# Optimization experiments

Measured on AMD Instinct MI355X. Metric: run time of the kernel, lower is better.

The kernel has to match this reference:

```python
import jax, jax.numpy as jnp
import numpy as np

D_MODEL = 2048
N_HEADS = 16
HEAD_DIM = 128
WINDOW = 512
ROPE_BASE = 10000.0
B, N = 2, 2048
INNER = N_HEADS * HEAD_DIM


def setup_inputs() -> dict:
    key = jax.random.key(0)
    k1, k2, k3 = jax.random.split(key, 3)
    x = jax.random.normal(k1, (B, N, D_MODEL), dtype=jnp.float32)
    # torch nn.Linear stores weight as [out_features, in_features]
    w_qkv = jax.random.normal(k2, (3 * INNER, D_MODEL), dtype=jnp.float32) / np.sqrt(D_MODEL)
    w_o = jax.random.normal(k3, (D_MODEL, INNER), dtype=jnp.float32) / np.sqrt(INNER)
    return {"x": x, "w_qkv": w_qkv, "w_o": w_o}


def _rotate_half(t):
    t1, t2 = jnp.split(t, 2, axis=-1)
    return jnp.concatenate([-t2, t1], axis=-1)


def _rope(q, k, offset=0):
    # q, k: [B, H, N, D]; GPT-NeoX half-split rotary embedding
    D = q.shape[-1]
    inv_freq = 1.0 / (ROPE_BASE ** (jnp.arange(0, D, 2, dtype=jnp.float32) / D))
    pos = jnp.arange(q.shape[2], dtype=jnp.float32) + offset
    ang = pos[:, None] * inv_freq[None, :]                 # [N, D/2]
    cos = jnp.concatenate([jnp.cos(ang), jnp.cos(ang)], axis=-1)  # [N, D]
    sin = jnp.concatenate([jnp.sin(ang), jnp.sin(ang)], axis=-1)
    q_r = q * cos + _rotate_half(q) * sin
    k_r = k * cos + _rotate_half(k) * sin
    return q_r, k_r


def reference(x, w_qkv, w_o):
    Bq, Nq, _ = x.shape
    # QKV projection (no bias)
    qkv = jnp.einsum('bnd,ed->bne', x, w_qkv)              # [B, N, 3*INNER]
    q, k, v = jnp.split(qkv, 3, axis=-1)
    def to_heads(t):
        return t.reshape(Bq, Nq, N_HEADS, HEAD_DIM).transpose(0, 2, 1, 3)  # [B,H,N,D]
    q, k, v = to_heads(q), to_heads(k), to_heads(v)
    q, k = _rope(q, k, offset=0)
    # sliding-window causal mask: valid key j for query i iff (i - WINDOW) < j <= i
    i = jnp.arange(Nq)[:, None]
    j = jnp.arange(Nq)[None, :]
    valid = (j > i - WINDOW) & (j <= i)                    # [N, N]
    scale = 1.0 / np.sqrt(HEAD_DIM)
    scores = jnp.einsum('bhnd,bhkd->bhnk', q, k) * scale   # [B,H,N,N]
    scores = jnp.where(valid[None, None], scores, -jnp.inf)
    att = jax.nn.softmax(scores, axis=-1)
    out = jnp.einsum('bhnk,bhkd->bhnd', att, v)
    out = out.transpose(0, 2, 1, 3).reshape(Bq, Nq, INNER)
    y = jnp.einsum('bni,di->bnd', out, w_o)
    return y
```

## Files before the change

### kernel.cpp

```cpp
#include <hip/hip_runtime.h>
#include <hip/hip_bf16.h>
#include <cstdint>

typedef __bf16 bf16x8 __attribute__((ext_vector_type(8)));
typedef float floatx4 __attribute__((ext_vector_type(4)));

__device__ __forceinline__ void gl2lds16(const void* g, void* l) {
  __builtin_amdgcn_global_load_lds(
      (const __attribute__((address_space(1))) unsigned int*)g,
      (__attribute__((address_space(3))) unsigned int*)(uintptr_t)l,
      16, 0, 0);
}

__global__ __launch_bounds__(256)
void cvt_kernel(const float* __restrict__ in, __hip_bfloat16* __restrict__ out, int n) {
  int i = (blockIdx.x * 256 + threadIdx.x) * 4;
  if (i >= n) return;
  const float4 v = *(const float4*)(in + i);
  out[i + 0] = __float2bfloat16(v.x);
  out[i + 1] = __float2bfloat16(v.y);
  out[i + 2] = __float2bfloat16(v.z);
  out[i + 3] = __float2bfloat16(v.w);
}

__global__ __launch_bounds__(256)
void cvt2_kernel(const float* __restrict__ in0, const float* __restrict__ in1,
                 __hip_bfloat16* __restrict__ out, int n0, int ntot) {
  int i = (blockIdx.x * 256 + threadIdx.x) * 4;
  if (i >= ntot) return;
  const float4 v = (i < n0) ? *(const float4*)(in0 + i)
                            : *(const float4*)(in1 + (i - n0));
  out[i + 0] = __float2bfloat16(v.x);
  out[i + 1] = __float2bfloat16(v.y);
  out[i + 2] = __float2bfloat16(v.z);
  out[i + 3] = __float2bfloat16(v.w);
}

#define MEMFENCE asm volatile("" ::: "memory")

__global__ __launch_bounds__(512, 2)
void gemm_qkv256(const __hip_bfloat16* __restrict__ A,
                 const __hip_bfloat16* __restrict__ W,
                 __hip_bfloat16* __restrict__ Qr,
                 __hip_bfloat16* __restrict__ Kr,
                 __hip_bfloat16* __restrict__ Vt)
{
  extern __shared__ __hip_bfloat16 sm[];
  const int tid = threadIdx.x, lane = tid & 63, wave = tid >> 6;
  const int wr = wave >> 2, wc = wave & 3;
  const int m0 = blockIdx.x << 8, n0 = blockIdx.y << 8;
  const int lrow = lane & 15, dg = lane >> 4, lq4 = dg * 4;
  const int rslot = (dg ^ ((lrow >> 1) & 3)) * 8;
  const int arow = tid >> 2;
  const int ascol = ((tid & 3) ^ ((tid >> 3) & 3)) * 8;
  const __hip_bfloat16* aS0 = A + (size_t)(m0 + arow) * 2048 + ascol;
  const __hip_bfloat16* aS1 = A + (size_t)(m0 + 128 + arow) * 2048 + ascol;
  const __hip_bfloat16* bS0 = W + (size_t)(n0 + arow) * 2048 + ascol;
  const __hip_bfloat16* bS1 = W + (size_t)(n0 + 128 + arow) * 2048 + ascol;
  floatx4 acc[8][4] = {};

#define QSTAGE(TT) do { const int bb_ = (TT) & 3; const int kk_ = (TT) * 32;   \
    gl2lds16(aS0 + kk_, &sm[bb_ * 16384 + tid * 8]);                           \
    gl2lds16(aS1 + kk_, &sm[bb_ * 16384 + 4096 + tid * 8]);                    \
    gl2lds16(bS0 + kk_, &sm[bb_ * 16384 + 8192 + tid * 8]);                    \
    gl2lds16(bS1 + kk_, &sm[bb_ * 16384 + 12288 + tid * 8]); } while (0)

#define QKSTEP(TT, WIMM, DOSTAGE) do {                                         \
    MEMFENCE; __builtin_amdgcn_s_waitcnt(WIMM); MEMFENCE;                      \
    __builtin_amdgcn_s_barrier(); MEMFENCE;                                    \
    const int bb = (TT) & 3;                                                   \
    if (DOSTAGE) QSTAGE((TT) + 3);                                             \
    bf16x8 af[8], bfr[4];                                                      \
    _Pragma("unroll")                                                          \
    for (int mt = 0; mt < 8; mt++)                                             \
      af[mt] = *(const bf16x8*)&sm[bb * 16384 + (wr * 128 + mt * 16 + lrow) * 32 + rslot]; \
    _Pragma("unroll")                                                          \
    for (int nt = 0; nt < 4; nt++)                                             \
      bfr[nt] = *(const bf16x8*)&sm[bb * 16384 + 8192 + (wc * 64 + nt * 16 + lrow) * 32 + rslot]; \
    __builtin_amdgcn_s_setprio(1);                                             \
    _Pragma("unroll")                                                          \
    for (int mt = 0; mt < 8; mt++)                                             \
      _Pragma("unroll")                                                        \
      for (int nt = 0; nt < 4; nt++)                                           \
        acc[mt][nt] = __builtin_amdgcn_mfma_f32_16x16x32_bf16(af[mt], bfr[nt], acc[mt][nt], 0, 0, 0); \
    __builtin_amdgcn_s_setprio(0);                                             \
  } while (0)

  QSTAGE(0); QSTAGE(1); QSTAGE(2);
  for (int t = 0; t < 61; ++t) QKSTEP(t, 0x0078, true);
  QKSTEP(61, 0x0078, false);
  QKSTEP(62, 0x0074, false);
  QKSTEP(63, 0x0070, false);
#undef QKSTEP
#undef QSTAGE

  const int seg = n0 >> 11;
  const int h0 = (n0 & 2047) >> 7;
  const int b = m0 >> 11;
  const int seq0 = m0 & 2047;
  float* invfp = (float*)((char*)sm + 122880);

  __syncthreads();
  if (seg < 2 && tid < 64) invfp[tid] = __expf(-(float)tid * 0.14391156831212787f);

  const float qs = (seg == 0) ? 0.08838834764831845f : 1.0f;
  for (int p = 0; p < 2; ++p) {
    if (p) __syncthreads();
    if (wr == p) {
      if (seg < 2) {
#pragma unroll
        for (int mt = 0; mt < 8; mt++)
#pragma unroll
          for (int nt = 0; nt < 4; nt++)
#pragma unroll
            for (int r = 0; r < 4; r++)
              sm[(mt * 16 + lq4 + r) * 264 + wc * 64 + nt * 16 + lrow] =
                  __float2bfloat16(acc[mt][nt][r]);
      } else {
#pragma unroll
        for (int mt = 0; mt < 8; mt++)
#pragma unroll
          for (int nt = 0; nt < 4; nt++)
#pragma unroll
            for (int r = 0; r < 4; r++)
              sm[(wc * 64 + nt * 16 + lrow) * 136 + mt * 16 + lq4 + r] =
                  __float2bfloat16(acc[mt][nt][r]);
      }
    }
    __syncthreads();
    if (seg < 2) {
      __hip_bfloat16* Out = seg ? Kr : Qr;
#pragma unroll
      for (int it = 0; it < 4; ++it) {
        const int task = tid + it * 512;
        const int row = task >> 4;
        const int hh = (task >> 3) & 1;
        const int g8 = (task & 7) * 8;
        const int seq = seq0 + p * 128 + row;
        const float pos = (float)seq;
        const bf16x8 lo8 = *(const bf16x8*)&sm[row * 264 + hh * 128 + g8];
        const bf16x8 hi8 = *(const bf16x8*)&sm[row * 264 + hh * 128 + g8 + 64];
        alignas(16) __hip_bfloat16 lo[8], hi[8];
#pragma unroll
        for (int k = 0; k < 8; k++) {
          float sn, cs;
          __sincosf(pos * invfp[g8 + k], &sn, &cs);
          const float a = (float)lo8[k];
          const float bb2 = (float)hi8[k];
          lo[k] = __float2bfloat16((a * cs - bb2 * sn) * qs);
          hi[k] = __float2bfloat16((bb2 * cs + a * sn) * qs);
        }
        const size_t ob = ((size_t)((b * 16 + h0 + hh) * 2048 + seq)) * 128;
        *(bf16x8*)&Out[ob + g8] = *(const bf16x8*)lo;
        *(bf16x8*)&Out[ob + g8 + 64] = *(const bf16x8*)hi;
      }
    } else {
#pragma unroll
      for (int it = 0; it < 8; ++it) {
        const int task = tid + it * 512;
        const int col = task >> 4;
        const int sg = (task & 15) * 8;
        const bf16x8 v8 = *(const bf16x8*)&sm[col * 136 + sg];
        const int hh = col >> 7, d = col & 127;
        *(bf16x8*)&Vt[((size_t)((b * 16 + h0 + hh) * 128 + d)) * 2048 + seq0 + p * 128 + sg] = v8;
      }
    }
  }
}

__global__ __launch_bounds__(512, 2)
void gemm_o256(const __hip_bfloat16* __restrict__ A,
               const __hip_bfloat16* __restrict__ Wo,
               float* __restrict__ C)
{
  extern __shared__ __hip_bfloat16 sm[];
  const int tid = threadIdx.x, lane = tid & 63, wave = tid >> 6;
  const int wr = wave >> 2, wc = wave & 3;
  const int m0 = blockIdx.x << 8, n0 = blockIdx.y << 7;
  const int lrow = lane & 15, dg = lane >> 4, lq4 = dg * 4;
  const int rslot = (dg ^ ((lrow >> 1) & 3)) * 8;
  const int arow = tid >> 2;
  const int ascol = ((tid & 3) ^ ((tid >> 3) & 3)) * 8;
  const __hip_bfloat16* aS0 = A + (size_t)(m0 + arow) * 2048 + ascol;
  const __hip_bfloat16* aS1 = A + (size_t)(m0 + 128 + arow) * 2048 + ascol;
  const __hip_bfloat16* bS0 = Wo + (size_t)(n0 + arow) * 2048 + ascol;
  floatx4 acc[8][2] = {};

#define OSTAGE(TT) do { const int bb_ = (TT) & 3; const int kk_ = (TT) * 32;   \
    gl2lds16(aS0 + kk_, &sm[bb_ * 12288 + tid * 8]);                           \
    gl2lds16(aS1 + kk_, &sm[bb_ * 12288 + 4096 + tid * 8]);                    \
    gl2lds16(bS0 + kk_, &sm[bb_ * 12288 + 8192 + tid * 8]); } while (0)

#define OKSTEP(TT, WIMM, DOSTAGE) do {                                         \
    MEMFENCE; __builtin_amdgcn_s_waitcnt(WIMM); MEMFENCE;                      \
    __builtin_amdgcn_s_barrier(); MEMFENCE;                                    \
    const int bb = (TT) & 3;                                                   \
    if (DOSTAGE) OSTAGE((TT) + 3);                                             \
    bf16x8 af[8], bfr[2];                                                      \
    _Pragma("unroll")                                                          \
    for (int mt = 0; mt < 8; mt++)                                             \
      af[mt] = *(const bf16x8*)&sm[bb * 12288 + (wr * 128 + mt * 16 + lrow) * 32 + rslot]; \
    _Pragma("unroll")                                                          \
    for (int nt = 0; nt < 2; nt++)                                             \
      bfr[nt] = *(const bf16x8*)&sm[bb * 12288 + 8192 + (wc * 32 + nt * 16 + lrow) * 32 + rslot]; \
    __builtin_amdgcn_s_setprio(1);                                             \
    _Pragma("unroll")                                                          \
    for (int mt = 0; mt < 8; mt++)                                             \
      _Pragma("unroll")                                                        \
      for (int nt = 0; nt < 2; nt++)                                           \
        acc[mt][nt] = __builtin_amdgcn_mfma_f32_16x16x32_bf16(af[mt], bfr[nt], acc[mt][nt], 0, 0, 0); \
    __builtin_amdgcn_s_setprio(0);                                             \
  } while (0)

  OSTAGE(0); OSTAGE(1); OSTAGE(2);
  for (int t = 0; t < 61; ++t) OKSTEP(t, 0x0076, true);
  OKSTEP(61, 0x0076, false);
  OKSTEP(62, 0x0073, false);
  OKSTEP(63, 0x0070, false);
#undef OKSTEP
#undef OSTAGE

#pragma unroll
  for (int mt = 0; mt < 8; mt++)
#pragma unroll
    for (int nt = 0; nt < 2; nt++)
#pragma unroll
      for (int r = 0; r < 4; r++)
        C[(size_t)(m0 + wr * 128 + mt * 16 + lq4 + r) * 2048 +
          (n0 + wc * 32 + nt * 16 + lrow)] = acc[mt][nt][r];
}

#define KSTR 136
#define VSTR 72
__global__ __launch_bounds__(512, 4)
void attn_swa(const __hip_bfloat16* __restrict__ Qr, const __hip_bfloat16* __restrict__ Kr,
              const __hip_bfloat16* __restrict__ Vt, __hip_bfloat16* __restrict__ Out)
{
  __shared__ __hip_bfloat16 Ks[64 * KSTR];
  __shared__ __hip_bfloat16 Vs[128 * VSTR];
  __shared__ __hip_bfloat16 Pb[8][16 * VSTR];
  const int qt = blockIdx.x, bh = blockIdx.y;
  const int tid = threadIdx.x, lane = tid & 63, wave = tid >> 6;
  const int lrow = lane & 15, lk = (lane >> 4) * 8, lq4 = (lane >> 4) * 4;
  const int i0 = qt * 128;
  const float NEG_INF = -__builtin_inff();
  const __hip_bfloat16* Qh = Qr + (size_t)bh * 2048 * 128;
  const __hip_bfloat16* Kh = Kr + (size_t)bh * 2048 * 128;
  const __hip_bfloat16* Vh = Vt + (size_t)bh * 128 * 2048;

  const int ck0 = tid, ck1 = tid + 512;
  const int kr0 = ck0 >> 4, kg0 = (ck0 & 15) * 8;
  const int kr1 = ck1 >> 4, kg1 = (ck1 & 15) * 8;
  const int cv0 = tid, cv1 = tid + 512;
  const int vd0 = cv0 >> 3, vc0 = (cv0 & 7) * 8;
  const int vd1 = cv1 >> 3, vc1 = (cv1 & 7) * 8;

  const int iw = i0 + wave * 16 + lrow;
  bf16x8 qf[4];
#pragma unroll
  for (int ks = 0; ks < 4; ks++)
    qf[ks] = *(const bf16x8*)&Qh[(size_t)iw * 128 + ks * 32 + lk];

  floatx4 accO[8] = {};
  float m_i = NEG_INF, l_i = 0.f;
  const int imin = i0 + wave * 16;
  const int lo = i0 - 511;
  const int jt_lo = (lo > 0 ? lo : 0) >> 6;
  const int jt_hi = (i0 + 127) >> 6;

  int j0n = jt_lo * 64;
  int4 rk0 = *(const int4*)&Kh[(size_t)(j0n + kr0) * 128 + kg0];
  int4 rk1 = *(const int4*)&Kh[(size_t)(j0n + kr1) * 128 + kg1];
  int4 rv0 = *(const int4*)&Vh[(size_t)vd0 * 2048 + j0n + vc0];
  int4 rv1 = *(const int4*)&Vh[(size_t)vd1 * 2048 + j0n + vc1];

  for (int jt = jt_lo; jt <= jt_hi; jt++) {
    const int j0 = jt * 64;
    __syncthreads();
    *(int4*)&Ks[kr0 * KSTR + kg0] = rk0;
    *(int4*)&Ks[kr1 * KSTR + kg1] = rk1;
    *(int4*)&Vs[vd0 * VSTR + vc0] = rv0;
    *(int4*)&Vs[vd1 * VSTR + vc1] = rv1;
    if (jt < jt_hi) {
      const int jn = j0 + 64;
      rk0 = *(const int4*)&Kh[(size_t)(jn + kr0) * 128 + kg0];
      rk1 = *(const int4*)&Kh[(size_t)(jn + kr1) * 128 + kg1];
      rv0 = *(const int4*)&Vh[(size_t)vd0 * 2048 + jn + vc0];
      rv1 = *(const int4*)&Vh[(size_t)vd1 * 2048 + jn + vc1];
    }
    asm volatile("" ::: "memory");
    __builtin_amdgcn_s_waitcnt(0xC07F);
    __builtin_amdgcn_s_barrier();
    asm volatile("" ::: "memory");

    floatx4 s[4] = {};
#pragma unroll
    for (int nt = 0; nt < 4; nt++) {
      const int krow = (nt * 16 + lrow) * KSTR;
#pragma unroll
      for (int ks = 0; ks < 4; ks++) {
        const bf16x8 kf = *(const bf16x8*)&Ks[krow + ks * 32 + lk];
        s[nt] = __builtin_amdgcn_mfma_f32_16x16x32_bf16(kf, qf[ks], s[nt], 0, 0, 0);
      }
    }
    const bool full = (j0 + 63 <= imin) && (j0 >= imin + 15 - 511);
    float rmax = NEG_INF;
    if (full) {
#pragma unroll
      for (int nt = 0; nt < 4; nt++)
#pragma unroll
        for (int r = 0; r < 4; r++) rmax = fmaxf(rmax, s[nt][r]);
    } else {
#pragma unroll
      for (int nt = 0; nt < 4; nt++) {
#pragma unroll
        for (int r = 0; r < 4; r++) {
          const int j = j0 + nt * 16 + lq4 + r;
          const float sv = ((j <= iw) && (j > iw - 512)) ? s[nt][r] : NEG_INF;
          s[nt][r] = sv;
          rmax = fmaxf(rmax, sv);
        }
      }
    }
    rmax = fmaxf(rmax, __shfl_xor(rmax, 16));
    rmax = fmaxf(rmax, __shfl_xor(rmax, 32));
    const float mnew = fmaxf(m_i, rmax);
    const float alpha = __expf(fminf(m_i - mnew, 0.f));
    m_i = mnew;
    float rs = 0.f;
    if (full) {
#pragma unroll
      for (int nt = 0; nt < 4; nt++)
#pragma unroll
        for (int r = 0; r < 4; r++) {
          const float p = __expf(s[nt][r] - mnew);
          s[nt][r] = p;
          rs += p;
        }
    } else {
#pragma unroll
      for (int nt = 0; nt < 4; nt++)
#pragma unroll
        for (int r = 0; r < 4; r++) {
          const float sv = s[nt][r];
          const float p = (sv == NEG_INF) ? 0.f : __expf(sv - mnew);
          s[nt][r] = p;
          rs += p;
        }
    }
    rs += __shfl_xor(rs, 16);
    rs += __shfl_xor(rs, 32);
    l_i = l_i * alpha + rs;
#pragma unroll
    for (int dt = 0; dt < 8; dt++) accO[dt] *= alpha;
#pragma unroll
    for (int nt = 0; nt < 4; nt++) {
      alignas(8) __hip_bfloat16 p4[4];
#pragma unroll
      for (int r = 0; r < 4; r++) p4[r] = __float2bfloat16(s[nt][r]);
      *(uint64_t*)&Pb[wave][lrow * VSTR + nt * 16 + lq4] = *(const uint64_t*)p4;
    }
    bf16x8 pf[2];
#pragma unroll
    for (int jf = 0; jf < 2; jf++)
      pf[jf] = *(const bf16x8*)&Pb[wave][lrow * VSTR + jf * 32 + lk];
#pragma unroll
    for (int dt = 0; dt < 8; dt++) {
      const int vrow = (dt * 16 + lrow) * VSTR;
#pragma unroll
      for (int jf = 0; jf < 2; jf++) {
        const bf16x8 vf = *(const bf16x8*)&Vs[vrow + jf * 32 + lk];
        accO[dt] = __builtin_amdgcn_mfma_f32_16x16x32_bf16(vf, pf[jf], accO[dt], 0, 0, 0);
      }
    }
  }
  const int b = bh >> 4, h = bh & 15;
  const float inv_l = 1.0f / l_i;
  const size_t rowb = ((size_t)(b * 2048 + iw)) * 2048 + h * 128;
#pragma unroll
  for (int dt = 0; dt < 8; dt++) {
    alignas(8) __hip_bfloat16 o4[4];
#pragma unroll
    for (int r = 0; r < 4; r++) o4[r] = __float2bfloat16(accO[dt][r] * inv_l);
    *(uint64_t*)&Out[rowb + dt * 16 + lq4] = *(const uint64_t*)o4;
  }
}

extern "C" void kernel_launch(void* const* d_in, const int* in_sizes, int n_in,
                              void* d_out, int out_size, void* d_ws, size_t ws_size,
                              hipStream_t stream)
{
  const float* x = (const float*)d_in[0];
  const float* w_qkv = (const float*)d_in[1];
  const float* w_o = (const float*)d_in[2];
  float* y = (float*)d_out;
  char* ws = (char*)d_ws;

  const size_t SZ_X = 16777216;
  const size_t SZ_WQKV = 25165824;
  const size_t SZ_Q = 16777216;

  __hip_bfloat16* xb = (__hip_bfloat16*)(ws);
  __hip_bfloat16* wqkvb = (__hip_bfloat16*)(ws + SZ_X);
  __hip_bfloat16* Qr = (__hip_bfloat16*)(ws + SZ_X + SZ_WQKV);
  __hip_bfloat16* Kr = (__hip_bfloat16*)(ws + SZ_X + SZ_WQKV + SZ_Q);
  __hip_bfloat16* Vt = (__hip_bfloat16*)(ws + SZ_X + SZ_WQKV + 2 * SZ_Q);

  static bool s_attr_done = false;
  if (!s_attr_done) {
    hipFuncSetAttribute((const void*)gemm_qkv256,
                        hipFuncAttributeMaxDynamicSharedMemorySize, 131072);
    hipFuncSetAttribute((const void*)gemm_o256,
                        hipFuncAttributeMaxDynamicSharedMemorySize, 98304);
    s_attr_done = true;
  }

  cvt2_kernel<<<dim3(20480), dim3(256), 0, stream>>>(x, w_qkv, xb, 8388608, 20971520);
  gemm_qkv256<<<dim3(16, 24), dim3(512), 131072, stream>>>(xb, wqkvb, Qr, Kr, Vt);
  attn_swa<<<dim3(16, 32), dim3(512), 0, stream>>>(Qr, Kr, Vt, xb );
  cvt_kernel<<<dim3(4096), dim3(256), 0, stream>>>(w_o, wqkvb, 4194304);
  gemm_o256<<<dim3(16, 16), dim3(512), 98304, stream>>>(xb, wqkvb, y);
}
```

Baseline: 338.9 us.

## Shrink QKV GEMM tile to 128x128 with swizzled block order and 3-stage pipeline

Rewrites the QKV projection GEMM from 256x256 tiles with 512 threads and a 4-stage LDS ring to 128x128 tiles with 256 threads and a 3-stage ring. Block IDs are remapped with an XCD-style swizzle for L2 locality, and the epilogue now handles a single head per block. The aim is more blocks (1536 instead of 384) and more resident blocks per CU, to fill the GPU better and reduce tail effects. The cost is lower arithmetic intensity per tile, so more global/L2 traffic for A and W.

```diff
diff --git a/kernel.cpp b/kernel.cpp
--- a/kernel.cpp
+++ b/kernel.cpp
@@ -38,8 +38,8 @@
 
 #define MEMFENCE asm volatile("" ::: "memory")
 
-__global__ __launch_bounds__(512, 2)
-void gemm_qkv256(const __hip_bfloat16* __restrict__ A,
+__global__ __launch_bounds__(256, 3)
+void gemm_qkv128(const __hip_bfloat16* __restrict__ A,
                  const __hip_bfloat16* __restrict__ W,
                  __hip_bfloat16* __restrict__ Qr,
                  __hip_bfloat16* __restrict__ Kr,
@@ -47,123 +47,118 @@
 {
   extern __shared__ __hip_bfloat16 sm[];
   const int tid = threadIdx.x, lane = tid & 63, wave = tid >> 6;
-  const int wr = wave >> 2, wc = wave & 3;
-  const int m0 = blockIdx.x << 8, n0 = blockIdx.y << 8;
+  const int wr = wave >> 1, wc = wave & 1;
+  const int bid = blockIdx.y * 32 + blockIdx.x;
+  const int swz = (bid & 7) * 192 + (bid >> 3);
+  const int m0 = (swz & 31) << 7;
+  const int n0 = (swz >> 5) << 7;
   const int lrow = lane & 15, dg = lane >> 4, lq4 = dg * 4;
   const int rslot = (dg ^ ((lrow >> 1) & 3)) * 8;
   const int arow = tid >> 2;
   const int ascol = ((tid & 3) ^ ((tid >> 3) & 3)) * 8;
   const __hip_bfloat16* aS0 = A + (size_t)(m0 + arow) * 2048 + ascol;
-  const __hip_bfloat16* aS1 = A + (size_t)(m0 + 128 + arow) * 2048 + ascol;
+  const __hip_bfloat16* aS1 = A + (size_t)(m0 + 64 + arow) * 2048 + ascol;
   const __hip_bfloat16* bS0 = W + (size_t)(n0 + arow) * 2048 + ascol;
-  const __hip_bfloat16* bS1 = W + (size_t)(n0 + 128 + arow) * 2048 + ascol;
-  floatx4 acc[8][4] = {};
-
-#define QSTAGE(TT) do { const int bb_ = (TT) & 3; const int kk_ = (TT) * 32;   \
-    gl2lds16(aS0 + kk_, &sm[bb_ * 16384 + tid * 8]);                           \
-    gl2lds16(aS1 + kk_, &sm[bb_ * 16384 + 4096 + tid * 8]);                    \
-    gl2lds16(bS0 + kk_, &sm[bb_ * 16384 + 8192 + tid * 8]);                    \
-    gl2lds16(bS1 + kk_, &sm[bb_ * 16384 + 12288 + tid * 8]); } while (0)
-
-#define QKSTEP(TT, WIMM, DOSTAGE) do {                                         \
-    MEMFENCE; __builtin_amdgcn_s_waitcnt(WIMM); MEMFENCE;                      \
-    __builtin_amdgcn_s_barrier(); MEMFENCE;                                    \
-    const int bb = (TT) & 3;                                                   \
-    if (DOSTAGE) QSTAGE((TT) + 3);                                             \
-    bf16x8 af[8], bfr[4];                                                      \
-    _Pragma("unroll")                                                          \
-    for (int mt = 0; mt < 8; mt++)                                             \
-      af[mt] = *(const bf16x8*)&sm[bb * 16384 + (wr * 128 + mt * 16 + lrow) * 32 + rslot]; \
+  const __hip_bfloat16* bS1 = W + (size_t)(n0 + 64 + arow) * 2048 + ascol;
+  float* invfp = (float*)((char*)sm + 49152);
+  if (tid < 64) invfp[tid] = __expf(-(float)tid * 0.14391156831212787f);
+  floatx4 acc[4][4] = {};
+
+#define QS128(TT) do { const int bo_ = ((TT) % 3) * 8192; const int kk_ = (TT) * 32; \
+    gl2lds16(aS0 + kk_, &sm[bo_ + tid * 8]);                                   \
+    gl2lds16(aS1 + kk_, &sm[bo_ + 2048 + tid * 8]);                            \
+    gl2lds16(bS0 + kk_, &sm[bo_ + 4096 + tid * 8]);                            \
+    gl2lds16(bS1 + kk_, &sm[bo_ + 6144 + tid * 8]); } while (0)
+
+#define QC128(BO) do {                                                         \
+    bf16x8 af[4], bfr[4];                                                      \
+    _Pragma("unroll")                                                          \
+    for (int mt = 0; mt < 4; mt++)                                             \
+      af[mt] = *(const bf16x8*)&sm[(BO) + (wr * 64 + mt * 16 + lrow) * 32 + rslot]; \
     _Pragma("unroll")                                                          \
     for (int nt = 0; nt < 4; nt++)                                             \
-      bfr[nt] = *(const bf16x8*)&sm[bb * 16384 + 8192 + (wc * 64 + nt * 16 + lrow) * 32 + rslot]; \
+      bfr[nt] = *(const bf16x8*)&sm[(BO) + 4096 + (wc * 64 + nt * 16 + lrow) * 32 + rslot]; \
     __builtin_amdgcn_s_setprio(1);                                             \
     _Pragma("unroll")                                                          \
-    for (int mt = 0; mt < 8; mt++)                                             \
+    for (int mt = 0; mt < 4; mt++)                                             \
       _Pragma("unroll")                                                        \
       for (int nt = 0; nt < 4; nt++)                                           \
         acc[mt][nt] = __builtin_amdgcn_mfma_f32_16x16x32_bf16(af[mt], bfr[nt], acc[mt][nt], 0, 0, 0); \
     __builtin_amdgcn_s_setprio(0);                                             \
   } while (0)
 
-  QSTAGE(0); QSTAGE(1); QSTAGE(2);
-  for (int t = 0; t < 61; ++t) QKSTEP(t, 0x0078, true);
-  QKSTEP(61, 0x0078, false);
-  QKSTEP(62, 0x0074, false);
-  QKSTEP(63, 0x0070, false);
-#undef QKSTEP
-#undef QSTAGE
+  QS128(0); QS128(1);
+  for (int t = 0; t < 63; ++t) {
+    MEMFENCE; __builtin_amdgcn_s_waitcnt(0x0074); MEMFENCE;
+    __builtin_amdgcn_s_barrier(); MEMFENCE;
+    if (t < 62) QS128(t + 2);
+    QC128((t % 3) * 8192);
+  }
+  MEMFENCE; __builtin_amdgcn_s_waitcnt(0x0070); MEMFENCE;
+  __builtin_amdgcn_s_barrier(); MEMFENCE;
+  QC128((63 % 3) * 8192);
+#undef QC128
+#undef QS128
 
   const int seg = n0 >> 11;
-  const int h0 = (n0 & 2047) >> 7;
+  const int h = (n0 & 2047) >> 7;
   const int b = m0 >> 11;
   const int seq0 = m0 & 2047;
-  float* invfp = (float*)((char*)sm + 122880);
-
   __syncthreads();
-  if (seg < 2 && tid < 64) invfp[tid] = __expf(-(float)tid * 0.14391156831212787f);
-
+  if (seg < 2) {
+#pragma unroll
+    for (int mt = 0; mt < 4; mt++)
+#pragma unroll
+      for (int nt = 0; nt < 4; nt++)
+#pragma unroll
+        for (int r = 0; r < 4; r++)
+          sm[(wr * 64 + mt * 16 + lq4 + r) * 136 + wc * 64 + nt * 16 + lrow] =
+              __float2bfloat16(acc[mt][nt][r]);
+  } else {
+#pragma unroll
+    for (int mt = 0; mt < 4; mt++)
+#pragma unroll
+      for (int nt = 0; nt < 4; nt++)
+#pragma unroll
+        for (int r = 0; r < 4; r++)
+          sm[(wc * 64 + nt * 16 + lrow) * 136 + wr * 64 + mt * 16 + lq4 + r] =
+              __float2bfloat16(acc[mt][nt][r]);
+  }
+  __syncthreads();
   const float qs = (seg == 0) ? 0.08838834764831845f : 1.0f;
-  for (int p = 0; p < 2; ++p) {
-    if (p) __syncthreads();
-    if (wr == p) {
-      if (seg < 2) {
-#pragma unroll
-        for (int mt = 0; mt < 8; mt++)
-#pragma unroll
-          for (int nt = 0; nt < 4; nt++)
-#pragma unroll
-            for (int r = 0; r < 4; r++)
-              sm[(mt * 16 + lq4 + r) * 264 + wc * 64 + nt * 16 + lrow] =
-                  __float2bfloat16(acc[mt][nt][r]);
-      } else {
-#pragma unroll
-        for (int mt = 0; mt < 8; mt++)
-#pragma unroll
-          for (int nt = 0; nt < 4; nt++)
-#pragma unroll
-            for (int r = 0; r < 4; r++)
-              sm[(wc * 64 + nt * 16 + lrow) * 136 + mt * 16 + lq4 + r] =
-                  __float2bfloat16(acc[mt][nt][r]);
+  if (seg < 2) {
+    __hip_bfloat16* Out = seg ? Kr : Qr;
+#pragma unroll
+    for (int it = 0; it < 4; ++it) {
+      const int task = tid + it * 256;
+      const int row = task >> 3;
+      const int g8 = (task & 7) * 8;
+      const int seq = seq0 + row;
+      const float pos = (float)seq;
+      const bf16x8 lo8 = *(const bf16x8*)&sm[row * 136 + g8];
+      const bf16x8 hi8 = *(const bf16x8*)&sm[row * 136 + g8 + 64];
+      alignas(16) __hip_bfloat16 lo[8], hi[8];
+#pragma unroll
+      for (int k = 0; k < 8; k++) {
+        float sn, cs;
+        __sincosf(pos * invfp[g8 + k], &sn, &cs);
+        const float a = (float)lo8[k];
+        const float bb2 = (float)hi8[k];
+        lo[k] = __float2bfloat16((a * cs - bb2 * sn) * qs);
+        hi[k] = __float2bfloat16((bb2 * cs + a * sn) * qs);
       }
-    }
-    __syncthreads();
-    if (seg < 2) {
-      __hip_bfloat16* Out = seg ? Kr : Qr;
-#pragma unroll
-      for (int it = 0; it < 4; ++it) {
-        const int task = tid + it * 512;
-        const int row = task >> 4;
-        const int hh = (task >> 3) & 1;
-        const int g8 = (task & 7) * 8;
-        const int seq = seq0 + p * 128 + row;
-        const float pos = (float)seq;
-        const bf16x8 lo8 = *(const bf16x8*)&sm[row * 264 + hh * 128 + g8];
-        const bf16x8 hi8 = *(const bf16x8*)&sm[row * 264 + hh * 128 + g8 + 64];
-        alignas(16) __hip_bfloat16 lo[8], hi[8];
-#pragma unroll
-        for (int k = 0; k < 8; k++) {
-          float sn, cs;
-          __sincosf(pos * invfp[g8 + k], &sn, &cs);
-          const float a = (float)lo8[k];
-          const float bb2 = (float)hi8[k];
-          lo[k] = __float2bfloat16((a * cs - bb2 * sn) * qs);
-          hi[k] = __float2bfloat16((bb2 * cs + a * sn) * qs);
-        }
-        const size_t ob = ((size_t)((b * 16 + h0 + hh) * 2048 + seq)) * 128;
-        *(bf16x8*)&Out[ob + g8] = *(const bf16x8*)lo;
-        *(bf16x8*)&Out[ob + g8 + 64] = *(const bf16x8*)hi;
-      }
-    } else {
-#pragma unroll
-      for (int it = 0; it < 8; ++it) {
-        const int task = tid + it * 512;
-        const int col = task >> 4;
-        const int sg = (task & 15) * 8;
-        const bf16x8 v8 = *(const bf16x8*)&sm[col * 136 + sg];
-        const int hh = col >> 7, d = col & 127;
-        *(bf16x8*)&Vt[((size_t)((b * 16 + h0 + hh) * 128 + d)) * 2048 + seq0 + p * 128 + sg] = v8;
-      }
+      const size_t ob = ((size_t)((b * 16 + h) * 2048 + seq)) * 128;
+      *(bf16x8*)&Out[ob + g8] = *(const bf16x8*)lo;
+      *(bf16x8*)&Out[ob + g8 + 64] = *(const bf16x8*)hi;
+    }
+  } else {
+#pragma unroll
+    for (int it = 0; it < 8; ++it) {
+      const int task = tid + it * 256;
+      const int col = task >> 4;
+      const int sg = (task & 15) * 8;
+      const bf16x8 v8 = *(const bf16x8*)&sm[col * 136 + sg];
+      *(bf16x8*)&Vt[((size_t)((b * 16 + h) * 128 + col)) * 2048 + seq0 + sg] = v8;
     }
   }
 }
@@ -408,15 +403,13 @@
 
   static bool s_attr_done = false;
   if (!s_attr_done) {
-    hipFuncSetAttribute((const void*)gemm_qkv256,
-                        hipFuncAttributeMaxDynamicSharedMemorySize, 131072);
     hipFuncSetAttribute((const void*)gemm_o256,
                         hipFuncAttributeMaxDynamicSharedMemorySize, 98304);
     s_attr_done = true;
   }
 
   cvt2_kernel<<<dim3(20480), dim3(256), 0, stream>>>(x, w_qkv, xb, 8388608, 20971520);
-  gemm_qkv256<<<dim3(16, 24), dim3(512), 131072, stream>>>(xb, wqkvb, Qr, Kr, Vt);
+  gemm_qkv128<<<dim3(32, 48), dim3(256), 49408, stream>>>(xb, wqkvb, Qr, Kr, Vt);
   attn_swa<<<dim3(16, 32), dim3(512), 0, stream>>>(Qr, Kr, Vt, xb );
   cvt_kernel<<<dim3(4096), dim3(256), 0, stream>>>(w_o, wqkvb, 4194304);
   gemm_o256<<<dim3(16, 16), dim3(512), 98304, stream>>>(xb, wqkvb, y);
```

Measured after the change: 357.9 us. 5.6% more time.
